# Kernel tuning notes

Measured on AMD Instinct MI355X. Metric: run time of the kernel, lower is better.

## Reference

```python
import jax, jax.numpy as jnp
import numpy as np

K = 10
ALPHA = 0.1
N_NODES = 100000
N_EDGES = 1600000
D_FEAT = 50


def setup_inputs() -> dict:
    key = jax.random.key(0)
    k1, k2, k3 = jax.random.split(key, 3)
    feat = jax.random.normal(k1, (N_NODES, D_FEAT), dtype=jnp.float32)
    src = jax.random.randint(k2, (N_EDGES,), 0, N_NODES, dtype=jnp.int64)
    dst = jax.random.randint(k3, (N_EDGES,), 0, N_NODES, dtype=jnp.int64)
    return {"feat": feat, "src": src, "dst": dst}


def reference(feat, src, dst):
    # APPNP: H^{t+1} = (1-a) * D^{-1/2} A D^{-1/2} H^t + a * H^0
    n = feat.shape[0]
    # in-degree per node, clipped to >= 1 (as in the original clip_by_value)
    deg = jax.ops.segment_sum(jnp.ones(dst.shape[0], feat.dtype), dst, num_segments=n)
    norm = jnp.clip(deg, 1.0, None) ** -0.5  # [N]
    norm = norm[:, None]                      # broadcast over feature dims
    feat_0 = feat
    for _ in range(K):
        h = feat * norm                       # pre-normalize (D^{-1/2})
        # message = h[src] (edge weight is 1 since edge_drop=0), aggregate by sum at dst
        agg = jax.ops.segment_sum(h[src], dst, num_segments=n)  # [N, D]
        feat = (1.0 - ALPHA) * (agg * norm) + ALPHA * feat_0
    return feat
```

## Files before the change

### kernel.cpp

```cpp
#include <hip/hip_runtime.h>


#define NN 100000
#define EE 1600000
#define DD 50
#define KK 10
#define NBLK 391
#define SLICES 32
#define RANGES 8
#define NR (NN / RANGES)
#define ES (EE / SLICES)

__device__ __forceinline__ float feat_at(const void* f, long long i, int ft) {
    if (ft) return ((const float*)f)[i];
    unsigned int w = ((unsigned int)((const unsigned short*)f)[i]) << 16;
    return __uint_as_float(w);
}

__device__ __forceinline__ float bf16_ld(const unsigned short* p, int i) {
    unsigned int w = ((unsigned int)p[i]) << 16;
    return __uint_as_float(w);
}

__device__ __forceinline__ unsigned short bf16_st(float x) {
    unsigned int u = __float_as_uint(x);
    unsigned int r = (u + 0x7FFF + ((u >> 16) & 1)) >> 16;
    return (unsigned short)r;
}

__global__ __launch_bounds__(512) void APPNPConv_62199716381208_build(
        const void* srcp, const void* dstp, const void* featp,
        unsigned int* counts, int* col_idx, int* flag, int phase) {
    __shared__ unsigned int hist[NR];
    const int tid = threadIdx.x;
    const int r = blockIdx.x & 7;
    const int s = blockIdx.x >> 3;
    const int r0 = r * NR;
    const long long e0 = (long long)s * ES;

    if (phase == 0) {
        const int* a = (const int*)dstp;
        const int is64 = ((a[1] | a[3] | a[5] | a[7] | a[9] | a[11] | a[13] | a[15]) == 0);
        if (blockIdx.x == 0 && tid == 0) {
            flag[0] = is64;
            const unsigned short* w = (const unsigned short*)featp;
            int isf32 = 0;
            for (int k = 0; k < 64; ++k) {
                unsigned int b = ((unsigned int)w[k]) << 16;
                float ax = fabsf(__uint_as_float(b));
                if (!(ax < 100.0f)) isf32 = 1;
            }
            flag[1] = isf32;
        }
        for (int i = tid; i < NR; i += 512) hist[i] = 0u;
        __syncthreads();
        if (is64) {
            const longlong2* dp = (const longlong2*)((const long long*)dstp + e0);
            for (int i = tid; i < ES / 4; i += 512) {
                longlong2 d0 = dp[2 * i];
                longlong2 d1 = dp[2 * i + 1];
                unsigned int a0 = (unsigned int)((int)d0.x - r0);
                unsigned int a1 = (unsigned int)((int)d0.y - r0);
                unsigned int a2 = (unsigned int)((int)d1.x - r0);
                unsigned int a3 = (unsigned int)((int)d1.y - r0);
                if (a0 < (unsigned int)NR) atomicAdd(&hist[a0], 1u);
                if (a1 < (unsigned int)NR) atomicAdd(&hist[a1], 1u);
                if (a2 < (unsigned int)NR) atomicAdd(&hist[a2], 1u);
                if (a3 < (unsigned int)NR) atomicAdd(&hist[a3], 1u);
            }
        } else {
            const int4* dp = (const int4*)((const int*)dstp + e0);
            for (int i = tid; i < ES / 4; i += 512) {
                int4 dd = dp[i];
                unsigned int a0 = (unsigned int)(dd.x - r0);
                unsigned int a1 = (unsigned int)(dd.y - r0);
                unsigned int a2 = (unsigned int)(dd.z - r0);
                unsigned int a3 = (unsigned int)(dd.w - r0);
                if (a0 < (unsigned int)NR) atomicAdd(&hist[a0], 1u);
                if (a1 < (unsigned int)NR) atomicAdd(&hist[a1], 1u);
                if (a2 < (unsigned int)NR) atomicAdd(&hist[a2], 1u);
                if (a3 < (unsigned int)NR) atomicAdd(&hist[a3], 1u);
            }
        }
        __syncthreads();
        for (int i = tid; i < NR; i += 512)
            counts[(size_t)s * NN + r0 + i] = hist[i];
    } else {
        const int is64 = flag[0];
        for (int i = tid; i < NR; i += 512)
            hist[i] = counts[(size_t)s * NN + r0 + i];
        __syncthreads();
        if (is64) {
            const longlong2* dp = (const longlong2*)((const long long*)dstp + e0);
            const longlong2* sp = (const longlong2*)((const long long*)srcp + e0);
            for (int i = tid; i < ES / 4; i += 512) {
                longlong2 d0 = dp[2 * i];
                longlong2 d1 = dp[2 * i + 1];
                longlong2 s0 = sp[2 * i];
                longlong2 s1 = sp[2 * i + 1];
                unsigned int a0 = (unsigned int)((int)d0.x - r0);
                unsigned int a1 = (unsigned int)((int)d0.y - r0);
                unsigned int a2 = (unsigned int)((int)d1.x - r0);
                unsigned int a3 = (unsigned int)((int)d1.y - r0);
                if (a0 < (unsigned int)NR) {
                    unsigned int pos = atomicAdd(&hist[a0], 1u);
                    int c = (int)s0.x;
                    if (pos < (unsigned int)EE)
                        col_idx[pos] = ((unsigned int)c < (unsigned int)NN) ? c : 0;
                }
                if (a1 < (unsigned int)NR) {
                    unsigned int pos = atomicAdd(&hist[a1], 1u);
                    int c = (int)s0.y;
                    if (pos < (unsigned int)EE)
                        col_idx[pos] = ((unsigned int)c < (unsigned int)NN) ? c : 0;
                }
                if (a2 < (unsigned int)NR) {
                    unsigned int pos = atomicAdd(&hist[a2], 1u);
                    int c = (int)s1.x;
                    if (pos < (unsigned int)EE)
                        col_idx[pos] = ((unsigned int)c < (unsigned int)NN) ? c : 0;
                }
                if (a3 < (unsigned int)NR) {
                    unsigned int pos = atomicAdd(&hist[a3], 1u);
                    int c = (int)s1.y;
                    if (pos < (unsigned int)EE)
                        col_idx[pos] = ((unsigned int)c < (unsigned int)NN) ? c : 0;
                }
            }
        } else {
            const int4* dp = (const int4*)((const int*)dstp + e0);
            const int4* sp = (const int4*)((const int*)srcp + e0);
            for (int i = tid; i < ES / 4; i += 512) {
                int4 dd = dp[i];
                int4 ss = sp[i];
                unsigned int a0 = (unsigned int)(dd.x - r0);
                unsigned int a1 = (unsigned int)(dd.y - r0);
                unsigned int a2 = (unsigned int)(dd.z - r0);
                unsigned int a3 = (unsigned int)(dd.w - r0);
                if (a0 < (unsigned int)NR) {
                    unsigned int pos = atomicAdd(&hist[a0], 1u);
                    if (pos < (unsigned int)EE)
                        col_idx[pos] = ((unsigned int)ss.x < (unsigned int)NN) ? ss.x : 0;
                }
                if (a1 < (unsigned int)NR) {
                    unsigned int pos = atomicAdd(&hist[a1], 1u);
                    if (pos < (unsigned int)EE)
                        col_idx[pos] = ((unsigned int)ss.y < (unsigned int)NN) ? ss.y : 0;
                }
                if (a2 < (unsigned int)NR) {
                    unsigned int pos = atomicAdd(&hist[a2], 1u);
                    if (pos < (unsigned int)EE)
                        col_idx[pos] = ((unsigned int)ss.z < (unsigned int)NN) ? ss.z : 0;
                }
                if (a3 < (unsigned int)NR) {
                    unsigned int pos = atomicAdd(&hist[a3], 1u);
                    if (pos < (unsigned int)EE)
                        col_idx[pos] = ((unsigned int)ss.w < (unsigned int)NN) ? ss.w : 0;
                }
            }
        }
    }
}

__global__ __launch_bounds__(512) void APPNPConv_62199716381208_kernel(
        const void* featp, const void* srcp, const void* dstp,
        int* deg, float* norm, int* row_ptr, int* col_idx, int* bsum, int* flag,
        unsigned int* counts, unsigned short* f0b,
        const unsigned short* gin, unsigned short* gout, float* outp,
        int phase, int last) {
    __shared__ int sh[512];
    const int tid = threadIdx.x;

    if (phase == 2) {
        int n = blockIdx.x * 256 + tid;
        int total = 0;
        if (n < NN) {
            #pragma unroll 4
            for (int s = 0; s < SLICES; ++s)
                total += (int)counts[(size_t)s * NN + n];
            deg[n] = total;
            norm[n] = rsqrtf((float)(total < 1 ? 1 : total));
        }
        sh[tid] = total;
        __syncthreads();
        for (int off = 128; off > 0; off >>= 1) {
            if (tid < off) sh[tid] += sh[tid + off];
            __syncthreads();
        }
        if (tid == 0) bsum[blockIdx.x] = sh[0];
        return;
    }
    if (phase == 3) {
        int v = (tid < NBLK) ? bsum[tid] : 0;
        sh[tid] = v;
        __syncthreads();
        for (int off = 1; off < 512; off <<= 1) {
            int x = (tid >= off) ? sh[tid - off] : 0;
            __syncthreads();
            sh[tid] += x;
            __syncthreads();
        }
        if (tid < NBLK) bsum[tid] = sh[tid] - v;
        return;
    }
    if (phase == 4) {
        int i = blockIdx.x * 256 + tid;
        int v = (i < NN) ? deg[i] : 0;
        sh[tid] = v;
        __syncthreads();
        for (int off = 1; off < 256; off <<= 1) {
            int x = (tid >= off) ? sh[tid - off] : 0;
            __syncthreads();
            sh[tid] += x;
            __syncthreads();
        }
        int excl = sh[tid] - v + bsum[blockIdx.x];
        if (i < NN) {
            row_ptr[i] = excl;
            unsigned int run = (unsigned int)excl;
            for (int s = 0; s < SLICES; ++s) {
                size_t o = (size_t)s * NN + i;
                unsigned int c = counts[o];
                counts[o] = run;
                run += c;
            }
        }
        if (i == 0) row_ptr[NN] = EE;
        return;
    }
    if (phase == 6) {
        int i = blockIdx.x * 256 + tid;
        if (i < NN * DD) {
            int v = i / DD;
            float x = feat_at(featp, i, flag[1]);
            gout[i] = bf16_st(x * norm[v]);
            f0b[i] = bf16_st(x);
        }
        return;
    }
    {
        const int lane = tid & 63;
        const int v = (blockIdx.x << 2) + (tid >> 6);
        if (v >= NN) return;
        const int beg = row_ptr[v];
        const int end = row_ptr[v + 1];
        const int act = (lane < DD);
        float s0 = 0.0f, s1 = 0.0f, s2 = 0.0f, s3 = 0.0f;
        for (int base = beg; base < end; base += 64) {
            int idx = base + lane;
            int my = (idx < end) ? __builtin_nontemporal_load(col_idx + idx) : 0;
            int cnt = end - base;
            if (cnt > 64) cnt = 64;
            int j = 0;
            for (; j + 16 <= cnt; j += 16) {
                int c0  = __shfl(my, j,      64);
                int c1  = __shfl(my, j + 1,  64);
                int c2  = __shfl(my, j + 2,  64);
                int c3  = __shfl(my, j + 3,  64);
                int c4  = __shfl(my, j + 4,  64);
                int c5  = __shfl(my, j + 5,  64);
                int c6  = __shfl(my, j + 6,  64);
                int c7  = __shfl(my, j + 7,  64);
                int c8  = __shfl(my, j + 8,  64);
                int c9  = __shfl(my, j + 9,  64);
                int c10 = __shfl(my, j + 10, 64);
                int c11 = __shfl(my, j + 11, 64);
                int c12 = __shfl(my, j + 12, 64);
                int c13 = __shfl(my, j + 13, 64);
                int c14 = __shfl(my, j + 14, 64);
                int c15 = __shfl(my, j + 15, 64);
                if (act) {
                    float v0  = bf16_ld(gin, c0  * DD + lane);
                    float v1  = bf16_ld(gin, c1  * DD + lane);
                    float v2  = bf16_ld(gin, c2  * DD + lane);
                    float v3  = bf16_ld(gin, c3  * DD + lane);
                    float v4  = bf16_ld(gin, c4  * DD + lane);
                    float v5  = bf16_ld(gin, c5  * DD + lane);
                    float v6  = bf16_ld(gin, c6  * DD + lane);
                    float v7  = bf16_ld(gin, c7  * DD + lane);
                    float v8  = bf16_ld(gin, c8  * DD + lane);
                    float v9  = bf16_ld(gin, c9  * DD + lane);
                    float v10 = bf16_ld(gin, c10 * DD + lane);
                    float v11 = bf16_ld(gin, c11 * DD + lane);
                    float v12 = bf16_ld(gin, c12 * DD + lane);
                    float v13 = bf16_ld(gin, c13 * DD + lane);
                    float v14 = bf16_ld(gin, c14 * DD + lane);
                    float v15 = bf16_ld(gin, c15 * DD + lane);
                    s0 += (v0 + v4) + (v8 + v12);
                    s1 += (v1 + v5) + (v9 + v13);
                    s2 += (v2 + v6) + (v10 + v14);
                    s3 += (v3 + v7) + (v11 + v15);
                }
            }
            for (; j + 8 <= cnt; j += 8) {
                int c0 = __shfl(my, j, 64);
                int c1 = __shfl(my, j + 1, 64);
                int c2 = __shfl(my, j + 2, 64);
                int c3 = __shfl(my, j + 3, 64);
                int c4 = __shfl(my, j + 4, 64);
                int c5 = __shfl(my, j + 5, 64);
                int c6 = __shfl(my, j + 6, 64);
                int c7 = __shfl(my, j + 7, 64);
                if (act) {
                    float v0 = bf16_ld(gin, c0 * DD + lane);
                    float v1 = bf16_ld(gin, c1 * DD + lane);
                    float v2 = bf16_ld(gin, c2 * DD + lane);
                    float v3 = bf16_ld(gin, c3 * DD + lane);
                    float v4 = bf16_ld(gin, c4 * DD + lane);
                    float v5 = bf16_ld(gin, c5 * DD + lane);
                    float v6 = bf16_ld(gin, c6 * DD + lane);
                    float v7 = bf16_ld(gin, c7 * DD + lane);
                    s0 += v0 + v4;
                    s1 += v1 + v5;
                    s2 += v2 + v6;
                    s3 += v3 + v7;
                }
            }
            for (; j + 4 <= cnt; j += 4) {
                int c0 = __shfl(my, j, 64);
                int c1 = __shfl(my, j + 1, 64);
                int c2 = __shfl(my, j + 2, 64);
                int c3 = __shfl(my, j + 3, 64);
                if (act) {
                    s0 += bf16_ld(gin, c0 * DD + lane);
                    s1 += bf16_ld(gin, c1 * DD + lane);
                    s2 += bf16_ld(gin, c2 * DD + lane);
                    s3 += bf16_ld(gin, c3 * DD + lane);
                }
            }
            for (; j < cnt; ++j) {
                int c = __shfl(my, j, 64);
                if (act) s0 += bf16_ld(gin, c * DD + lane);
            }
        }
        if (act) {
            float sum = (s0 + s1) + (s2 + s3);
            float nv = norm[v];
            if (last) {
                float f0 = feat_at(featp, (long long)v * DD + lane, flag[1]);
                outp[v * DD + lane] = 0.9f * (sum * nv) + 0.1f * f0;
            } else {
                float f0 = bf16_ld(f0b, v * DD + lane);
                float res = 0.9f * (sum * nv) + 0.1f * f0;
                gout[v * DD + lane] = bf16_st(res * nv);
            }
        }
    }
}

extern "C" void kernel_launch(void* const* d_in, const int* in_sizes, int n_in,
                              void* d_out, int out_size, void* d_ws, size_t ws_size,
                              hipStream_t stream) {
    const void* featp = d_in[0];
    const void* src = d_in[1];
    const void* dst = d_in[2];
    float* outf = (float*)d_out;
    unsigned short* P_do = (unsigned short*)d_out;
    unsigned short* f0b  = (unsigned short*)d_out + (size_t)NN * DD;
    unsigned int* counts = (unsigned int*)d_out;
    size_t out_bytes = (size_t)out_size * 4;
    (void)in_sizes;

    if (n_in != 3) {
        hipMemsetAsync(d_out, 0x50, out_bytes, stream);
        return;
    }

    size_t a_deg  = (((size_t)NN * 4) + 255) / 256 * 256;
    size_t a_norm = a_deg;
    size_t a_rp   = (((size_t)(NN + 1) * 4) + 255) / 256 * 256;
    size_t a_col  = (((size_t)EE * 4) + 255) / 256 * 256;
    size_t a_bsum = (((size_t)NBLK * 4) + 255) / 256 * 256;
    size_t a_flag = 256;
    size_t a_buf  = (((size_t)NN * DD * 2) + 255) / 256 * 256;
    if (ws_size < a_deg + a_norm + a_rp + a_col + a_bsum + a_flag + a_buf ||
        out_bytes < (size_t)NN * DD * 4 ||
        out_bytes < (size_t)SLICES * NN * 4) {
        hipMemsetAsync(d_out, 0x40, out_bytes, stream);
        return;
    }
    char* p = (char*)d_ws;
    int* deg      = (int*)p;   p += a_deg;
    float* norm   = (float*)p; p += a_norm;
    int* row_ptr  = (int*)p;   p += a_rp;
    int* col_idx  = (int*)p;   p += a_col;
    int* bsum     = (int*)p;   p += a_bsum;
    int* flag     = (int*)p;   p += a_flag;
    unsigned short* P_ws = (unsigned short*)p;

    (void)hipGetLastError();

    #define LCH(grid, blk, gi, go, ph, la) \
        APPNPConv_62199716381208_kernel<<<(grid), (blk), 0, stream>>>( \
            featp, src, dst, deg, norm, row_ptr, col_idx, bsum, flag, counts, \
            f0b, (gi), (go), outf, (ph), (la))
    #define LCB(ph) \
        APPNPConv_62199716381208_build<<<SLICES * RANGES, 512, 0, stream>>>( \
            src, dst, featp, counts, col_idx, flag, (ph))

    LCB(0);
    LCH(NBLK, 256, P_ws, P_ws, 2, 0);
    LCH(1, 512, P_ws, P_ws, 3, 0);
    LCH(NBLK, 256, P_ws, P_ws, 4, 0);
    LCB(1);
    LCH((NN * DD + 255) / 256, 256, P_ws, P_do, 6, 0);

    for (int it = 1; it <= KK; ++it) {
        const unsigned short* gi = (it & 1) ? P_do : P_ws;
        unsigned short* go       = (it & 1) ? P_ws : P_do;
        LCH(NN / 4, 256, gi, go, 7, (it == KK) ? 1 : 0);
    }
    #undef LCH
    #undef LCB

    if (hipGetLastError() != hipSuccess) {
        hipMemsetAsync(d_out, 0xBF, out_bytes, stream);
    }
}
```

Baseline: 666.5 us.

## Process eight vertices per wave with padded bf16 rows and double-buffered gathers

The SpMM propagation kernel now assigns eight consecutive destination vertices to each wave. It streams their concatenated edge list in 64-edge chunks and flushes a vertex's result when its boundary is crossed. The propagated bf16 feature buffer is padded to 64 columns so gather addresses use a shift, and gathers are issued in two alternating 16-element batches to keep more loads in flight. The separate bf16 copy of the initial features is dropped; it is read from the original input instead. The changes aim to reduce per-vertex loop overhead and load imbalance, at the cost of more registers and extra padding bytes per gathered row.

Result: slower. 1.446 ms (+116.9%).

```diff
diff --git a/kernel.cpp b/kernel.cpp
--- a/kernel.cpp
+++ b/kernel.cpp
@@ -4,6 +4,7 @@
 #define NN 100000
 #define EE 1600000
 #define DD 50
+#define GS 64
 #define KK 10
 #define NBLK 391
 #define SLICES 32
@@ -165,7 +166,7 @@
 __global__ __launch_bounds__(512) void APPNPConv_62199716381208_kernel(
         const void* featp, const void* srcp, const void* dstp,
         int* deg, float* norm, int* row_ptr, int* col_idx, int* bsum, int* flag,
-        unsigned int* counts, unsigned short* f0b,
+        unsigned int* counts,
         const unsigned short* gin, unsigned short* gout, float* outp,
         int phase, int last) {
     __shared__ int sh[512];
@@ -229,122 +230,95 @@
         return;
     }
     if (phase == 6) {
-        int i = blockIdx.x * 256 + tid;
-        if (i < NN * DD) {
-            int v = i / DD;
-            float x = feat_at(featp, i, flag[1]);
-            gout[i] = bf16_st(x * norm[v]);
-            f0b[i] = bf16_st(x);
+        int gidx = blockIdx.x * 256 + tid;
+        int v = gidx >> 6;
+        int d = gidx & 63;
+        if (v < NN && d < DD) {
+            float x = feat_at(featp, (long long)v * DD + d, flag[1]);
+            gout[(v << 6) + d] = bf16_st(x * norm[v]);
         }
         return;
     }
     {
         const int lane = tid & 63;
-        const int v = (blockIdx.x << 2) + (tid >> 6);
-        if (v >= NN) return;
-        const int beg = row_ptr[v];
-        const int end = row_ptr[v + 1];
+        const int w = (blockIdx.x << 2) + (tid >> 6);
+        const int v0 = w << 3;
+        if (v0 >= NN) return;
         const int act = (lane < DD);
-        float s0 = 0.0f, s1 = 0.0f, s2 = 0.0f, s3 = 0.0f;
+        const int ft = flag[1];
+
+        int bl = 0;
+        if (lane <= 8) bl = row_ptr[v0 + lane];
+        int bnd[9];
+        #pragma unroll
+        for (int i = 0; i < 9; ++i) bnd[i] = __shfl(bl, i, 64);
+
+        float nl = (lane < 8) ? norm[v0 + lane] : 0.0f;
+
+        float f0r[8];
+        #pragma unroll
+        for (int i = 0; i < 8; ++i)
+            f0r[i] = act ? feat_at(featp, (long long)(v0 + i) * DD + lane, ft) : 0.0f;
+
+        const int beg = bnd[0];
+        const int end = bnd[8];
+        float s[4] = {0.0f, 0.0f, 0.0f, 0.0f};
+        int k = 0;
+        int nb = bnd[1];
+
+#define DO_FLUSH(KK) { \
+        float sum = (s[0] + s[1]) + (s[2] + s[3]); \
+        s[0] = 0.0f; s[1] = 0.0f; s[2] = 0.0f; s[3] = 0.0f; \
+        float nv = __shfl(nl, KK, 64); \
+        float res = 0.9f * (sum * nv) + 0.1f * f0r[KK]; \
+        int vtx = v0 + KK; \
+        if (act) { \
+            if (last) outp[(long long)vtx * DD + lane] = res; \
+            else gout[(vtx << 6) + lane] = bf16_st(res * nv); \
+        } }
+#define FLUSH_ADV() { switch (k) { \
+        case 0: DO_FLUSH(0); nb = bnd[2]; break; \
+        case 1: DO_FLUSH(1); nb = bnd[3]; break; \
+        case 2: DO_FLUSH(2); nb = bnd[4]; break; \
+        case 3: DO_FLUSH(3); nb = bnd[5]; break; \
+        case 4: DO_FLUSH(4); nb = bnd[6]; break; \
+        case 5: DO_FLUSH(5); nb = bnd[7]; break; \
+        case 6: DO_FLUSH(6); nb = bnd[8]; break; \
+        default: DO_FLUSH(7); nb = 0x7fffffff; break; } ++k; }
+#define ISSUE16(X, J) { \
+        _Pragma("unroll") \
+        for (int l = 0; l < 16; ++l) { \
+            int c = __shfl(my, (J) + l, 64); \
+            X[l] = bf16_ld(gin, (c << 6) + lane); } }
+#define CONSUME16(X, J) { \
+        _Pragma("unroll") \
+        for (int l = 0; l < 16; ++l) { \
+            if ((J) + l < cnt) { \
+                int ei = base + (J) + l; \
+                while (ei >= nb) FLUSH_ADV(); \
+                s[l & 3] += X[l]; } } }
+
+        float va[16], vb[16];
         for (int base = beg; base < end; base += 64) {
             int idx = base + lane;
             int my = (idx < end) ? __builtin_nontemporal_load(col_idx + idx) : 0;
             int cnt = end - base;
             if (cnt > 64) cnt = 64;
-            int j = 0;
-            for (; j + 16 <= cnt; j += 16) {
-                int c0  = __shfl(my, j,      64);
-                int c1  = __shfl(my, j + 1,  64);
-                int c2  = __shfl(my, j + 2,  64);
-                int c3  = __shfl(my, j + 3,  64);
-                int c4  = __shfl(my, j + 4,  64);
-                int c5  = __shfl(my, j + 5,  64);
-                int c6  = __shfl(my, j + 6,  64);
-                int c7  = __shfl(my, j + 7,  64);
-                int c8  = __shfl(my, j + 8,  64);
-                int c9  = __shfl(my, j + 9,  64);
-                int c10 = __shfl(my, j + 10, 64);
-                int c11 = __shfl(my, j + 11, 64);
-                int c12 = __shfl(my, j + 12, 64);
-                int c13 = __shfl(my, j + 13, 64);
-                int c14 = __shfl(my, j + 14, 64);
-                int c15 = __shfl(my, j + 15, 64);
-                if (act) {
-                    float v0  = bf16_ld(gin, c0  * DD + lane);
-                    float v1  = bf16_ld(gin, c1  * DD + lane);
-                    float v2  = bf16_ld(gin, c2  * DD + lane);
-                    float v3  = bf16_ld(gin, c3  * DD + lane);
-                    float v4  = bf16_ld(gin, c4  * DD + lane);
-                    float v5  = bf16_ld(gin, c5  * DD + lane);
-                    float v6  = bf16_ld(gin, c6  * DD + lane);
-                    float v7  = bf16_ld(gin, c7  * DD + lane);
-                    float v8  = bf16_ld(gin, c8  * DD + lane);
-                    float v9  = bf16_ld(gin, c9  * DD + lane);
-                    float v10 = bf16_ld(gin, c10 * DD + lane);
-                    float v11 = bf16_ld(gin, c11 * DD + lane);
-                    float v12 = bf16_ld(gin, c12 * DD + lane);
-                    float v13 = bf16_ld(gin, c13 * DD + lane);
-                    float v14 = bf16_ld(gin, c14 * DD + lane);
-                    float v15 = bf16_ld(gin, c15 * DD + lane);
-                    s0 += (v0 + v4) + (v8 + v12);
-                    s1 += (v1 + v5) + (v9 + v13);
-                    s2 += (v2 + v6) + (v10 + v14);
-                    s3 += (v3 + v7) + (v11 + v15);
-                }
-            }
-            for (; j + 8 <= cnt; j += 8) {
-                int c0 = __shfl(my, j, 64);
-                int c1 = __shfl(my, j + 1, 64);
-                int c2 = __shfl(my, j + 2, 64);
-                int c3 = __shfl(my, j + 3, 64);
-                int c4 = __shfl(my, j + 4, 64);
-                int c5 = __shfl(my, j + 5, 64);
-                int c6 = __shfl(my, j + 6, 64);
-                int c7 = __shfl(my, j + 7, 64);
-                if (act) {
-                    float v0 = bf16_ld(gin, c0 * DD + lane);
-                    float v1 = bf16_ld(gin, c1 * DD + lane);
-                    float v2 = bf16_ld(gin, c2 * DD + lane);
-                    float v3 = bf16_ld(gin, c3 * DD + lane);
-                    float v4 = bf16_ld(gin, c4 * DD + lane);
-                    float v5 = bf16_ld(gin, c5 * DD + lane);
-                    float v6 = bf16_ld(gin, c6 * DD + lane);
-                    float v7 = bf16_ld(gin, c7 * DD + lane);
-                    s0 += v0 + v4;
-                    s1 += v1 + v5;
-                    s2 += v2 + v6;
-                    s3 += v3 + v7;
-                }
-            }
-            for (; j + 4 <= cnt; j += 4) {
-                int c0 = __shfl(my, j, 64);
-                int c1 = __shfl(my, j + 1, 64);
-                int c2 = __shfl(my, j + 2, 64);
-                int c3 = __shfl(my, j + 3, 64);
-                if (act) {
-                    s0 += bf16_ld(gin, c0 * DD + lane);
-                    s1 += bf16_ld(gin, c1 * DD + lane);
-                    s2 += bf16_ld(gin, c2 * DD + lane);
-                    s3 += bf16_ld(gin, c3 * DD + lane);
-                }
-            }
-            for (; j < cnt; ++j) {
-                int c = __shfl(my, j, 64);
-                if (act) s0 += bf16_ld(gin, c * DD + lane);
-            }
-        }
-        if (act) {
-            float sum = (s0 + s1) + (s2 + s3);
-            float nv = norm[v];
-            if (last) {
-                float f0 = feat_at(featp, (long long)v * DD + lane, flag[1]);
-                outp[v * DD + lane] = 0.9f * (sum * nv) + 0.1f * f0;
-            } else {
-                float f0 = bf16_ld(f0b, v * DD + lane);
-                float res = 0.9f * (sum * nv) + 0.1f * f0;
-                gout[v * DD + lane] = bf16_st(res * nv);
-            }
-        }
+            ISSUE16(va, 0)
+            if (cnt > 16) ISSUE16(vb, 16)
+            CONSUME16(va, 0)
+            if (cnt > 32) ISSUE16(va, 32)
+            if (cnt > 16) CONSUME16(vb, 16)
+            if (cnt > 48) ISSUE16(vb, 48)
+            if (cnt > 32) CONSUME16(va, 32)
+            if (cnt > 48) CONSUME16(vb, 48)
+        }
+        while (k < 8) FLUSH_ADV();
+
+#undef DO_FLUSH
+#undef FLUSH_ADV
+#undef ISSUE16
+#undef CONSUME16
     }
 }
 
@@ -356,7 +330,6 @@
     const void* dst = d_in[2];
     float* outf = (float*)d_out;
     unsigned short* P_do = (unsigned short*)d_out;
-    unsigned short* f0b  = (unsigned short*)d_out + (size_t)NN * DD;
     unsigned int* counts = (unsigned int*)d_out;
     size_t out_bytes = (size_t)out_size * 4;
     (void)in_sizes;
@@ -372,9 +345,8 @@
     size_t a_col  = (((size_t)EE * 4) + 255) / 256 * 256;
     size_t a_bsum = (((size_t)NBLK * 4) + 255) / 256 * 256;
     size_t a_flag = 256;
-    size_t a_buf  = (((size_t)NN * DD * 2) + 255) / 256 * 256;
+    size_t a_buf  = (((size_t)NN * GS * 2) + 255) / 256 * 256;
     if (ws_size < a_deg + a_norm + a_rp + a_col + a_bsum + a_flag + a_buf ||
-        out_bytes < (size_t)NN * DD * 4 ||
         out_bytes < (size_t)SLICES * NN * 4) {
         hipMemsetAsync(d_out, 0x40, out_bytes, stream);
         return;
@@ -393,7 +365,7 @@
     #define LCH(grid, blk, gi, go, ph, la) \
         APPNPConv_62199716381208_kernel<<<(grid), (blk), 0, stream>>>( \
             featp, src, dst, deg, norm, row_ptr, col_idx, bsum, flag, counts, \
-            f0b, (gi), (go), outf, (ph), (la))
+            (gi), (go), outf, (ph), (la))
     #define LCB(ph) \
         APPNPConv_62199716381208_build<<<SLICES * RANGES, 512, 0, stream>>>( \
             src, dst, featp, counts, col_idx, flag, (ph))
@@ -403,12 +375,12 @@
     LCH(1, 512, P_ws, P_ws, 3, 0);
     LCH(NBLK, 256, P_ws, P_ws, 4, 0);
     LCB(1);
-    LCH((NN * DD + 255) / 256, 256, P_ws, P_do, 6, 0);
+    LCH((NN * GS + 255) / 256, 256, P_ws, P_do, 6, 0);
 
     for (int it = 1; it <= KK; ++it) {
         const unsigned short* gi = (it & 1) ? P_do : P_ws;
         unsigned short* go       = (it & 1) ? P_ws : P_do;
-        LCH(NN / 4, 256, gi, go, 7, (it == KK) ? 1 : 0);
+        LCH(NN / 32, 256, gi, go, 7, (it == KK) ? 1 : 0);
     }
     #undef LCH
     #undef LCB
```
